# Optimization experiments

Measured on AMD Instinct MI355X. Metric: run time of the kernel, lower is better.

Reference implementation:

```python
import jax, jax.numpy as jnp
import numpy as np

B, S, D, H = 4, 2048, 768, 12
HD = D // H  # head_dim = 64


def setup_inputs() -> dict:
    key = jax.random.key(0)
    k1, k2, k3, k4, k5 = jax.random.split(key, 5)
    scale = 0.02
    return {
        "x": jax.random.normal(k1, (B, S, D), dtype=jnp.float32),
        "w_qkv": jax.random.normal(k2, (D, 3 * D), dtype=jnp.float32) * scale,
        "b_qkv": jax.random.normal(k3, (3 * D,), dtype=jnp.float32) * scale,
        "w_proj": jax.random.normal(k4, (D, D), dtype=jnp.float32) * scale,
        "b_proj": jax.random.normal(k5, (D,), dtype=jnp.float32) * scale,
    }


def reference(x, w_qkv, b_qkv, w_proj, b_proj):
    b, s, d = x.shape
    # fused qkv projection: (b, s, 3d) -> (3, b, h, s, hd)
    qkv = x @ w_qkv + b_qkv
    qkv = qkv.reshape(b, s, 3, H, HD).transpose(2, 0, 3, 1, 4)
    q, k, v = qkv[0], qkv[1], qkv[2]
    # scaled dot-product attention with explicit (b, h, s, s) scores
    scores = jnp.einsum("bhqd,bhkd->bhqk", q, k) / jnp.sqrt(jnp.float32(HD))
    attn = jax.nn.softmax(scores, axis=-1)
    out = jnp.einsum("bhqk,bhkd->bhqd", attn, v)
    out = out.transpose(0, 2, 1, 3).reshape(b, s, d)  # concat heads
    return out @ w_proj + b_proj
```

## Files before the change

### kernel.cpp

```cpp
#include <hip/hip_runtime.h>
#include <hip/hip_bf16.h>
#include <stdint.h>


typedef __attribute__((ext_vector_type(8))) short bf16x8;
typedef __attribute__((ext_vector_type(4))) float f32x4;
typedef __attribute__((ext_vector_type(4))) unsigned short u16x4;

__device__ __forceinline__ unsigned short f2bf(float x) {
  union { float f; uint32_t u; } v; v.f = x;
  uint32_t r = v.u + 0x7FFF + ((v.u >> 16) & 1);
  return (unsigned short)(r >> 16);
}

__device__ __forceinline__ uint32_t cvtpk_bf16(float lo, float hi) {
  uint32_t r;
  asm("v_cvt_pk_bf16_f32 %0, %1, %2" : "=v"(r) : "v"(lo), "v"(hi));
  return r;
}

__device__ __forceinline__ void gload_lds16(const void* g, void* l) {
  __builtin_amdgcn_global_load_lds(
      (const __attribute__((address_space(1))) void*)g,
      (__attribute__((address_space(3))) void*)l, 16, 0, 0);
}

__global__ void cast_x_kernel(const float* __restrict__ x,
                              unsigned short* __restrict__ xb, int n) {
  int idx = (blockIdx.x * blockDim.x + threadIdx.x) * 4;
  if (idx < n) {
    f32x4 v = *(const f32x4*)(x + idx);
    u16x4 o;
    o[0] = f2bf(v[0]); o[1] = f2bf(v[1]); o[2] = f2bf(v[2]); o[3] = f2bf(v[3]);
    *(u16x4*)(xb + idx) = o;
  }
}

__global__ void transpose_cast_kernel(const float* __restrict__ W,
                                      unsigned short* __restrict__ Wt,
                                      int K, int N) {
  __shared__ float tile[64][65];
  int k0 = blockIdx.y * 64, n0 = blockIdx.x * 64;
  int t = threadIdx.x;
#pragma unroll
  for (int i = 0; i < 16; i++) {
    int idx = i * 256 + t; int r = idx >> 6, c = idx & 63;
    tile[r][c] = W[(size_t)(k0 + r) * N + n0 + c];
  }
  __syncthreads();
#pragma unroll
  for (int i = 0; i < 16; i++) {
    int idx = i * 256 + t; int r = idx >> 6, c = idx & 63;
    Wt[(size_t)(n0 + r) * K + k0 + c] = f2bf(tile[c][r]);
  }
}

template <int EPI>
__global__ __launch_bounds__(256, 2) void gemm_kernel(
    const unsigned short* __restrict__ A,
    const unsigned short* __restrict__ Bt,
    const float* __restrict__ bias,
    void* __restrict__ out0,
    unsigned short* __restrict__ Kb,
    unsigned short* __restrict__ Vt,
    int M, int N, int K) {
  __shared__ unsigned short As[128 * 64];
  __shared__ unsigned short Bs[128 * 64];
  const int tid = threadIdx.x;
  const int wave = tid >> 6, lane = tid & 63;
  const int wm = wave >> 1, wn = wave & 1;
  int m0, n0;
  if (EPI == 0) {
    const int id = blockIdx.x;
    const int xcd = id & 7, slot = id >> 3;
    m0 = (xcd * 8 + slot / 18) * 128;
    n0 = (slot % 18) * 128;
  } else {
    m0 = blockIdx.y * 128;
    n0 = blockIdx.x * 128;
  }
  const int g = lane >> 4, c16 = lane & 15;
  f32x4 acc[4][4] = {};

  for (int k0 = 0; k0 < K; k0 += 64) {
    int rb = wave * 32;
#pragma unroll
    for (int j = 0; j < 4; j++) {
      int r = rb + j * 8 + (lane >> 3);
      int ca = (lane & 7) ^ (r & 7);
      gload_lds16(A + (size_t)(m0 + r) * K + k0 + ca * 8, As + (rb + j * 8) * 64);
      gload_lds16(Bt + (size_t)(n0 + r) * K + k0 + ca * 8, Bs + (rb + j * 8) * 64);
    }
    __syncthreads();
#pragma unroll
    for (int ks = 0; ks < 2; ks++) {
      bf16x8 af[4], bfr[4];
#pragma unroll
      for (int mi = 0; mi < 4; mi++) {
        int row = wm * 64 + mi * 16 + c16;
        int ch = (ks * 4 + g) ^ (row & 7);
        af[mi] = *(const bf16x8*)(As + row * 64 + ch * 8);
      }
#pragma unroll
      for (int nj = 0; nj < 4; nj++) {
        int row = wn * 64 + nj * 16 + c16;
        int ch = (ks * 4 + g) ^ (row & 7);
        bfr[nj] = *(const bf16x8*)(Bs + row * 64 + ch * 8);
      }
#pragma unroll
      for (int mi = 0; mi < 4; mi++)
#pragma unroll
        for (int nj = 0; nj < 4; nj++)
          acc[mi][nj] = __builtin_amdgcn_mfma_f32_16x16x32_bf16(
              af[mi], bfr[nj], acc[mi][nj], 0, 0, 0);
    }
    __syncthreads();
  }

  if (EPI == 0) {
    const float QSC = 0.125f * 1.44269504088896f;
    unsigned short* Qb = (unsigned short*)out0;
#pragma unroll
    for (int nj = 0; nj < 4; nj++) {
      int n = n0 + wn * 64 + nj * 16 + c16;
      int t = n / 768, rr = n % 768;
      int h = rr >> 6, d = rr & 63;
      float bv = bias[n];
#pragma unroll
      for (int mi = 0; mi < 4; mi++) {
        int mrow = m0 + wm * 64 + mi * 16 + g * 4;
        int b = mrow >> 11, s = mrow & 2047;
        if (t == 0) {
          size_t base = ((size_t)(b * 12 + h) * 2048 + s) * 64 + d;
#pragma unroll
          for (int rg = 0; rg < 4; rg++)
            Qb[base + (size_t)rg * 64] = f2bf((acc[mi][nj][rg] + bv) * QSC);
        } else if (t == 1) {
          size_t base = ((size_t)(b * 12 + h) * 2048 + s) * 64 + d;
#pragma unroll
          for (int rg = 0; rg < 4; rg++)
            Kb[base + (size_t)rg * 64] = f2bf(acc[mi][nj][rg] + bv);
        } else {
          int sp = (s & ~31) + (((s >> 2) & 3) << 3) + (((s >> 4) & 1) << 2);
          u16x4 p;
          p[0] = f2bf(acc[mi][nj][0] + bv);
          p[1] = f2bf(acc[mi][nj][1] + bv);
          p[2] = f2bf(acc[mi][nj][2] + bv);
          p[3] = f2bf(acc[mi][nj][3] + bv);
          *(u16x4*)(Vt + ((size_t)(b * 12 + h) * 64 + d) * 2048 + sp) = p;
        }
      }
    }
  } else {
    float* outp = (float*)out0;
#pragma unroll
    for (int nj = 0; nj < 4; nj++) {
      int n = n0 + wn * 64 + nj * 16 + c16;
      float bv = bias[n];
#pragma unroll
      for (int mi = 0; mi < 4; mi++) {
        int mrow = m0 + wm * 64 + mi * 16 + g * 4;
#pragma unroll
        for (int rg = 0; rg < 4; rg++)
          outp[(size_t)(mrow + rg) * N + n] = acc[mi][nj][rg] + bv;
      }
    }
  }
}

__global__ __launch_bounds__(256, 4) void attn_kernel(
    const unsigned short* __restrict__ Qb,
    const unsigned short* __restrict__ Kb,
    const unsigned short* __restrict__ Vt,
    unsigned short* __restrict__ Ao) {
  __shared__ unsigned short Ks[64 * 64];
  __shared__ unsigned short Vs[64 * 64];
  const int id = blockIdx.x;
  const int xcd = id & 7, slot = id >> 3;
  const int bh = xcd * 6 + (slot % 6);
  const int q0 = (slot / 6) * 128;
  const int tid = threadIdx.x;
  const int wave = tid >> 6, lane = tid & 63;
  const int g = lane >> 4, c16 = lane & 15;
  const int rw = c16 & 7;
  const int rb = wave * 16;

  const int sr = rb + (lane >> 3);
  const int sca = (lane & 7) ^ (sr & 7);
  const unsigned short* kp = Kb + ((size_t)bh * 2048 + sr) * 64 + sca * 8;
  const unsigned short* vp = Vt + ((size_t)bh * 64 + sr) * 2048 + sca * 8;

  bf16x8 qf[2][2];
  {
    const unsigned short* qp =
        Qb + ((size_t)bh * 2048 + q0 + wave * 32 + c16) * 64;
#pragma unroll
    for (int qa = 0; qa < 2; qa++) {
      qf[qa][0] = *(const bf16x8*)(qp + qa * 1024 + g * 8);
      qf[qa][1] = *(const bf16x8*)(qp + qa * 1024 + 32 + g * 8);
    }
  }
  f32x4 acc_o[2][4] = {};
  float l_run[2] = {0.f, 0.f};
  const int alane = (lane & 48) + g * 4;

  for (int kt = 0; kt < 32; kt++) {
    gload_lds16(kp, Ks + rb * 64);
    gload_lds16(kp + 8 * 64, Ks + (rb + 8) * 64);
    gload_lds16(vp, Vs + rb * 64);
    gload_lds16(vp + 8 * 2048, Vs + (rb + 8) * 64);
    kp += 64 * 64;
    vp += 64;
    __syncthreads();

    f32x4 sacc[2][4] = {};
#pragma unroll
    for (int ks = 0; ks < 2; ks++) {
#pragma unroll
      for (int nf = 0; nf < 4; nf++) {
        int row = nf * 16 + c16;
        int ch = (ks * 4 + g) ^ (row & 7);
        bf16x8 kf = *(const bf16x8*)(Ks + row * 64 + ch * 8);
        sacc[0][nf] =
            __builtin_amdgcn_mfma_f32_16x16x32_bf16(kf, qf[0][ks], sacc[0][nf], 0, 0, 0);
        sacc[1][nf] =
            __builtin_amdgcn_mfma_f32_16x16x32_bf16(kf, qf[1][ks], sacc[1][nf], 0, 0, 0);
      }
    }

#pragma unroll
    for (int qa = 0; qa < 2; qa++) {
      float rs = 0.f;
#pragma unroll
      for (int nf = 0; nf < 4; nf++) {
        sacc[qa][nf][0] = __builtin_amdgcn_exp2f(sacc[qa][nf][0]);
        sacc[qa][nf][1] = __builtin_amdgcn_exp2f(sacc[qa][nf][1]);
        sacc[qa][nf][2] = __builtin_amdgcn_exp2f(sacc[qa][nf][2]);
        sacc[qa][nf][3] = __builtin_amdgcn_exp2f(sacc[qa][nf][3]);
        rs += (sacc[qa][nf][0] + sacc[qa][nf][1]) +
              (sacc[qa][nf][2] + sacc[qa][nf][3]);
      }
      l_run[qa] += rs;
    }

#pragma unroll
    for (int ks = 0; ks < 2; ks++) {
      union { uint32_t w[4]; bf16x8 v8; } pa0, pa1;
      pa0.w[0] = cvtpk_bf16(sacc[0][2 * ks][0], sacc[0][2 * ks][1]);
      pa0.w[1] = cvtpk_bf16(sacc[0][2 * ks][2], sacc[0][2 * ks][3]);
      pa0.w[2] = cvtpk_bf16(sacc[0][2 * ks + 1][0], sacc[0][2 * ks + 1][1]);
      pa0.w[3] = cvtpk_bf16(sacc[0][2 * ks + 1][2], sacc[0][2 * ks + 1][3]);
      pa1.w[0] = cvtpk_bf16(sacc[1][2 * ks][0], sacc[1][2 * ks][1]);
      pa1.w[1] = cvtpk_bf16(sacc[1][2 * ks][2], sacc[1][2 * ks][3]);
      pa1.w[2] = cvtpk_bf16(sacc[1][2 * ks + 1][0], sacc[1][2 * ks + 1][1]);
      pa1.w[3] = cvtpk_bf16(sacc[1][2 * ks + 1][2], sacc[1][2 * ks + 1][3]);
#pragma unroll
      for (int nf = 0; nf < 4; nf++) {
        int row = nf * 16 + c16;
        int ch = (ks * 4 + g) ^ rw;
        bf16x8 vf = *(const bf16x8*)(&Vs[row * 64 + ch * 8]);
        acc_o[0][nf] =
            __builtin_amdgcn_mfma_f32_16x16x32_bf16(pa0.v8, vf, acc_o[0][nf], 0, 0, 0);
        acc_o[1][nf] =
            __builtin_amdgcn_mfma_f32_16x16x32_bf16(pa1.v8, vf, acc_o[1][nf], 0, 0, 0);
      }
    }
    __syncthreads();
  }

  const int b = bh / 12, h = bh % 12;
#pragma unroll
  for (int qa = 0; qa < 2; qa++) {
    float t = l_run[qa];
    t += __shfl_xor(t, 16);
    t += __shfl_xor(t, 32);
    float l_q[4];
#pragma unroll
    for (int rg = 0; rg < 4; rg++)
      l_q[rg] = __shfl(t, alane + rg);
#pragma unroll
    for (int nf = 0; nf < 4; nf++) {
#pragma unroll
      for (int rg = 0; rg < 4; rg++) {
        float v = acc_o[qa][nf][rg] / l_q[rg];
        int srow = q0 + wave * 32 + qa * 16 + g * 4 + rg;
        Ao[((size_t)(b * 2048 + srow)) * 768 + h * 64 + nf * 16 + c16] = f2bf(v);
      }
    }
  }
}

extern "C" void kernel_launch(void* const* d_in, const int* in_sizes, int n_in,
                              void* d_out, int out_size, void* d_ws, size_t ws_size,
                              hipStream_t stream) {
  const float* x      = (const float*)d_in[0];
  const float* w_qkv  = (const float*)d_in[1];
  const float* b_qkv  = (const float*)d_in[2];
  const float* w_proj = (const float*)d_in[3];
  const float* b_proj = (const float*)d_in[4];

  unsigned short* xb  = (unsigned short*)d_ws;
  unsigned short* wqt = xb + 6291456;
  unsigned short* wpt = wqt + 1769472;
  unsigned short* Qb  = wpt + 589824;
  unsigned short* Kb  = Qb + 6291456;
  unsigned short* Vt  = Kb + 6291456;
  unsigned short* Ao  = Vt + 6291456;

  cast_x_kernel<<<6144, 256, 0, stream>>>(x, xb, 6291456);
  transpose_cast_kernel<<<dim3(36, 12), 256, 0, stream>>>(w_qkv, wqt, 768, 2304);
  transpose_cast_kernel<<<dim3(12, 12), 256, 0, stream>>>(w_proj, wpt, 768, 768);

  gemm_kernel<0><<<1152, 256, 0, stream>>>(
      xb, wqt, b_qkv, (void*)Qb, Kb, Vt, 8192, 2304, 768);

  attn_kernel<<<768, 256, 0, stream>>>(Qb, Kb, Vt, Ao);

  gemm_kernel<1><<<dim3(6, 64), 256, 0, stream>>>(
      Ao, wpt, b_proj, d_out, nullptr, nullptr, 8192, 768, 768);
}
```

Measured before the change: 140.7 us.

## Merge prep kernels, XCD-swizzle projection GEMM, process two KV tiles per sync

Combines the input cast and both weight transpose-casts into one launch so the three prep kernels become one. The output projection GEMM now uses a 1D grid with an XCD-aware block mapping so that blocks sharing rows of A land on the same XCD. The attention loop loads two 64-row K/V tiles into doubled LDS buffers per iteration and processes both before syncing, which halves the barriers. The extra LDS may lower occupancy, and the loads are still not overlapped with compute.

```diff
diff --git a/kernel.cpp b/kernel.cpp
--- a/kernel.cpp
+++ b/kernel.cpp
@@ -25,33 +25,45 @@
       (__attribute__((address_space(3))) void*)l, 16, 0, 0);
 }
 
-__global__ void cast_x_kernel(const float* __restrict__ x,
-                              unsigned short* __restrict__ xb, int n) {
-  int idx = (blockIdx.x * blockDim.x + threadIdx.x) * 4;
-  if (idx < n) {
+__device__ __forceinline__ void transpose_tile(const float* __restrict__ W,
+                                               unsigned short* __restrict__ Wt,
+                                               int K, int N, int k0, int n0,
+                                               float (*tile)[65], int t) {
+#pragma unroll
+  for (int i = 0; i < 16; i++) {
+    int idx = i * 256 + t; int r = idx >> 6, c = idx & 63;
+    tile[r][c] = W[(size_t)(k0 + r) * N + n0 + c];
+  }
+  __syncthreads();
+#pragma unroll
+  for (int i = 0; i < 16; i++) {
+    int idx = i * 256 + t; int r = idx >> 6, c = idx & 63;
+    Wt[(size_t)(n0 + r) * K + k0 + c] = f2bf(tile[c][r]);
+  }
+}
+
+__global__ void prep_kernel(const float* __restrict__ x,
+                            unsigned short* __restrict__ xb,
+                            const float* __restrict__ w_qkv,
+                            unsigned short* __restrict__ wqt,
+                            const float* __restrict__ w_proj,
+                            unsigned short* __restrict__ wpt) {
+  __shared__ float tile[64][65];
+  const int id = blockIdx.x, t = threadIdx.x;
+  if (id < 6144) {
+    int idx = (id * 256 + t) * 4;
     f32x4 v = *(const f32x4*)(x + idx);
     u16x4 o;
     o[0] = f2bf(v[0]); o[1] = f2bf(v[1]); o[2] = f2bf(v[2]); o[3] = f2bf(v[3]);
     *(u16x4*)(xb + idx) = o;
-  }
-}
-
-__global__ void transpose_cast_kernel(const float* __restrict__ W,
-                                      unsigned short* __restrict__ Wt,
-                                      int K, int N) {
-  __shared__ float tile[64][65];
-  int k0 = blockIdx.y * 64, n0 = blockIdx.x * 64;
-  int t = threadIdx.x;
-#pragma unroll
-  for (int i = 0; i < 16; i++) {
-    int idx = i * 256 + t; int r = idx >> 6, c = idx & 63;
-    tile[r][c] = W[(size_t)(k0 + r) * N + n0 + c];
-  }
-  __syncthreads();
-#pragma unroll
-  for (int i = 0; i < 16; i++) {
-    int idx = i * 256 + t; int r = idx >> 6, c = idx & 63;
-    Wt[(size_t)(n0 + r) * K + k0 + c] = f2bf(tile[c][r]);
+  } else if (id < 6576) {
+    int tid = id - 6144;
+    transpose_tile(w_qkv, wqt, 768, 2304, (tid / 36) * 64, (tid % 36) * 64,
+                   tile, t);
+  } else {
+    int tid = id - 6576;
+    transpose_tile(w_proj, wpt, 768, 768, (tid / 12) * 64, (tid % 12) * 64,
+                   tile, t);
   }
 }
 
@@ -69,15 +81,15 @@
   const int tid = threadIdx.x;
   const int wave = tid >> 6, lane = tid & 63;
   const int wm = wave >> 1, wn = wave & 1;
+  const int id = blockIdx.x;
+  const int xcd = id & 7, slot = id >> 3;
   int m0, n0;
   if (EPI == 0) {
-    const int id = blockIdx.x;
-    const int xcd = id & 7, slot = id >> 3;
     m0 = (xcd * 8 + slot / 18) * 128;
     n0 = (slot % 18) * 128;
   } else {
-    m0 = blockIdx.y * 128;
-    n0 = blockIdx.x * 128;
+    m0 = (xcd * 8 + slot / 6) * 128;
+    n0 = (slot % 6) * 128;
   }
   const int g = lane >> 4, c16 = lane & 15;
   f32x4 acc[4][4] = {};
@@ -173,8 +185,8 @@
     const unsigned short* __restrict__ Kb,
     const unsigned short* __restrict__ Vt,
     unsigned short* __restrict__ Ao) {
-  __shared__ unsigned short Ks[64 * 64];
-  __shared__ unsigned short Vs[64 * 64];
+  __shared__ unsigned short Ks[2][64 * 64];
+  __shared__ unsigned short Vs[2][64 * 64];
   const int id = blockIdx.x;
   const int xcd = id & 7, slot = id >> 3;
   const int bh = xcd * 6 + (slot % 6);
@@ -204,65 +216,73 @@
   float l_run[2] = {0.f, 0.f};
   const int alane = (lane & 48) + g * 4;
 
-  for (int kt = 0; kt < 32; kt++) {
-    gload_lds16(kp, Ks + rb * 64);
-    gload_lds16(kp + 8 * 64, Ks + (rb + 8) * 64);
-    gload_lds16(vp, Vs + rb * 64);
-    gload_lds16(vp + 8 * 2048, Vs + (rb + 8) * 64);
-    kp += 64 * 64;
-    vp += 64;
+  for (int kt2 = 0; kt2 < 16; kt2++) {
+#pragma unroll
+    for (int bufi = 0; bufi < 2; bufi++) {
+      const unsigned short* kpb = kp + bufi * 64 * 64;
+      const unsigned short* vpb = vp + bufi * 64;
+      gload_lds16(kpb, &Ks[bufi][rb * 64]);
+      gload_lds16(kpb + 8 * 64, &Ks[bufi][(rb + 8) * 64]);
+      gload_lds16(vpb, &Vs[bufi][rb * 64]);
+      gload_lds16(vpb + 8 * 2048, &Vs[bufi][(rb + 8) * 64]);
+    }
+    kp += 2 * 64 * 64;
+    vp += 128;
     __syncthreads();
 
-    f32x4 sacc[2][4] = {};
-#pragma unroll
-    for (int ks = 0; ks < 2; ks++) {
-#pragma unroll
-      for (int nf = 0; nf < 4; nf++) {
-        int row = nf * 16 + c16;
-        int ch = (ks * 4 + g) ^ (row & 7);
-        bf16x8 kf = *(const bf16x8*)(Ks + row * 64 + ch * 8);
-        sacc[0][nf] =
-            __builtin_amdgcn_mfma_f32_16x16x32_bf16(kf, qf[0][ks], sacc[0][nf], 0, 0, 0);
-        sacc[1][nf] =
-            __builtin_amdgcn_mfma_f32_16x16x32_bf16(kf, qf[1][ks], sacc[1][nf], 0, 0, 0);
-      }
-    }
-
-#pragma unroll
-    for (int qa = 0; qa < 2; qa++) {
-      float rs = 0.f;
-#pragma unroll
-      for (int nf = 0; nf < 4; nf++) {
-        sacc[qa][nf][0] = __builtin_amdgcn_exp2f(sacc[qa][nf][0]);
-        sacc[qa][nf][1] = __builtin_amdgcn_exp2f(sacc[qa][nf][1]);
-        sacc[qa][nf][2] = __builtin_amdgcn_exp2f(sacc[qa][nf][2]);
-        sacc[qa][nf][3] = __builtin_amdgcn_exp2f(sacc[qa][nf][3]);
-        rs += (sacc[qa][nf][0] + sacc[qa][nf][1]) +
-              (sacc[qa][nf][2] + sacc[qa][nf][3]);
-      }
-      l_run[qa] += rs;
-    }
-
-#pragma unroll
-    for (int ks = 0; ks < 2; ks++) {
-      union { uint32_t w[4]; bf16x8 v8; } pa0, pa1;
-      pa0.w[0] = cvtpk_bf16(sacc[0][2 * ks][0], sacc[0][2 * ks][1]);
-      pa0.w[1] = cvtpk_bf16(sacc[0][2 * ks][2], sacc[0][2 * ks][3]);
-      pa0.w[2] = cvtpk_bf16(sacc[0][2 * ks + 1][0], sacc[0][2 * ks + 1][1]);
-      pa0.w[3] = cvtpk_bf16(sacc[0][2 * ks + 1][2], sacc[0][2 * ks + 1][3]);
-      pa1.w[0] = cvtpk_bf16(sacc[1][2 * ks][0], sacc[1][2 * ks][1]);
-      pa1.w[1] = cvtpk_bf16(sacc[1][2 * ks][2], sacc[1][2 * ks][3]);
-      pa1.w[2] = cvtpk_bf16(sacc[1][2 * ks + 1][0], sacc[1][2 * ks + 1][1]);
-      pa1.w[3] = cvtpk_bf16(sacc[1][2 * ks + 1][2], sacc[1][2 * ks + 1][3]);
-#pragma unroll
-      for (int nf = 0; nf < 4; nf++) {
-        int row = nf * 16 + c16;
-        int ch = (ks * 4 + g) ^ rw;
-        bf16x8 vf = *(const bf16x8*)(&Vs[row * 64 + ch * 8]);
-        acc_o[0][nf] =
-            __builtin_amdgcn_mfma_f32_16x16x32_bf16(pa0.v8, vf, acc_o[0][nf], 0, 0, 0);
-        acc_o[1][nf] =
-            __builtin_amdgcn_mfma_f32_16x16x32_bf16(pa1.v8, vf, acc_o[1][nf], 0, 0, 0);
+#pragma unroll
+    for (int bufi = 0; bufi < 2; bufi++) {
+      f32x4 sacc[2][4] = {};
+#pragma unroll
+      for (int ks = 0; ks < 2; ks++) {
+#pragma unroll
+        for (int nf = 0; nf < 4; nf++) {
+          int row = nf * 16 + c16;
+          int ch = (ks * 4 + g) ^ (row & 7);
+          bf16x8 kf = *(const bf16x8*)(&Ks[bufi][row * 64 + ch * 8]);
+          sacc[0][nf] = __builtin_amdgcn_mfma_f32_16x16x32_bf16(
+              kf, qf[0][ks], sacc[0][nf], 0, 0, 0);
+          sacc[1][nf] = __builtin_amdgcn_mfma_f32_16x16x32_bf16(
+              kf, qf[1][ks], sacc[1][nf], 0, 0, 0);
+        }
+      }
+
+#pragma unroll
+      for (int qa = 0; qa < 2; qa++) {
+        float rs = 0.f;
+#pragma unroll
+        for (int nf = 0; nf < 4; nf++) {
+          sacc[qa][nf][0] = __builtin_amdgcn_exp2f(sacc[qa][nf][0]);
+          sacc[qa][nf][1] = __builtin_amdgcn_exp2f(sacc[qa][nf][1]);
+          sacc[qa][nf][2] = __builtin_amdgcn_exp2f(sacc[qa][nf][2]);
+          sacc[qa][nf][3] = __builtin_amdgcn_exp2f(sacc[qa][nf][3]);
+          rs += (sacc[qa][nf][0] + sacc[qa][nf][1]) +
+                (sacc[qa][nf][2] + sacc[qa][nf][3]);
+        }
+        l_run[qa] += rs;
+      }
+
+#pragma unroll
+      for (int ks = 0; ks < 2; ks++) {
+        union { uint32_t w[4]; bf16x8 v8; } pa0, pa1;
+        pa0.w[0] = cvtpk_bf16(sacc[0][2 * ks][0], sacc[0][2 * ks][1]);
+        pa0.w[1] = cvtpk_bf16(sacc[0][2 * ks][2], sacc[0][2 * ks][3]);
+        pa0.w[2] = cvtpk_bf16(sacc[0][2 * ks + 1][0], sacc[0][2 * ks + 1][1]);
+        pa0.w[3] = cvtpk_bf16(sacc[0][2 * ks + 1][2], sacc[0][2 * ks + 1][3]);
+        pa1.w[0] = cvtpk_bf16(sacc[1][2 * ks][0], sacc[1][2 * ks][1]);
+        pa1.w[1] = cvtpk_bf16(sacc[1][2 * ks][2], sacc[1][2 * ks][3]);
+        pa1.w[2] = cvtpk_bf16(sacc[1][2 * ks + 1][0], sacc[1][2 * ks + 1][1]);
+        pa1.w[3] = cvtpk_bf16(sacc[1][2 * ks + 1][2], sacc[1][2 * ks + 1][3]);
+#pragma unroll
+        for (int nf = 0; nf < 4; nf++) {
+          int row = nf * 16 + c16;
+          int ch = (ks * 4 + g) ^ rw;
+          bf16x8 vf = *(const bf16x8*)(&Vs[bufi][row * 64 + ch * 8]);
+          acc_o[0][nf] = __builtin_amdgcn_mfma_f32_16x16x32_bf16(
+              pa0.v8, vf, acc_o[0][nf], 0, 0, 0);
+          acc_o[1][nf] = __builtin_amdgcn_mfma_f32_16x16x32_bf16(
+              pa1.v8, vf, acc_o[1][nf], 0, 0, 0);
+        }
       }
     }
     __syncthreads();
@@ -307,15 +327,13 @@
   unsigned short* Vt  = Kb + 6291456;
   unsigned short* Ao  = Vt + 6291456;
 
-  cast_x_kernel<<<6144, 256, 0, stream>>>(x, xb, 6291456);
-  transpose_cast_kernel<<<dim3(36, 12), 256, 0, stream>>>(w_qkv, wqt, 768, 2304);
-  transpose_cast_kernel<<<dim3(12, 12), 256, 0, stream>>>(w_proj, wpt, 768, 768);
+  prep_kernel<<<6720, 256, 0, stream>>>(x, xb, w_qkv, wqt, w_proj, wpt);
 
   gemm_kernel<0><<<1152, 256, 0, stream>>>(
       xb, wqt, b_qkv, (void*)Qb, Kb, Vt, 8192, 2304, 768);
 
   attn_kernel<<<768, 256, 0, stream>>>(Qb, Kb, Vt, Ao);
 
-  gemm_kernel<1><<<dim3(6, 64), 256, 0, stream>>>(
+  gemm_kernel<1><<<384, 256, 0, stream>>>(
       Ao, wpt, b_proj, d_out, nullptr, nullptr, 8192, 768, 768);
 }
```

After: 147.7 us. 4.9% more time.
